# Kernel tuning notes

Measured on AMD Instinct MI355X. Metric: run time of the kernel, lower is better.

The kernel has to match this reference:

```python
import jax, jax.numpy as jnp
import numpy as np

F_IN, U, N_CLS = 256, 512, 50


def _gru_scan(x_tbf, W, Uk, b):
    """Keras GRU (reset_after=True, tanh/sigmoid). x_tbf: [T,B,F]. Returns [T,B,U]."""
    b_in, b_rec = b[0], b[1]                 # each [3U]
    xg = jnp.einsum('tbf,fg->tbg', x_tbf, W) + b_in   # precompute input gates [T,B,3U]
    B = x_tbf.shape[1]
    h0 = jnp.zeros((B, U), dtype=x_tbf.dtype)

    def step(h, xt):
        rec = h @ Uk + b_rec                 # [B,3U]
        xz, xr, xh = jnp.split(xt, 3, axis=-1)
        rz, rr, rh = jnp.split(rec, 3, axis=-1)
        z = jax.nn.sigmoid(xz + rz)
        r = jax.nn.sigmoid(xr + rr)
        hh = jnp.tanh(xh + r * rh)
        h_new = z * h + (1.0 - z) * hh
        return h_new, h_new

    _, ys = jax.lax.scan(step, h0, xg)
    return ys


def setup_inputs() -> dict:
    key = jax.random.key(0)
    ks = jax.random.split(key, 10)
    x = jax.random.normal(ks[0], (32, 1024, F_IN), dtype=jnp.float32)
    # glorot-ish scales
    s_w = (2.0 / (F_IN + 3 * U)) ** 0.5
    s_u = (2.0 / (U + 3 * U)) ** 0.5
    s_d = (2.0 / (2 * U + N_CLS)) ** 0.5
    Wf = jax.random.normal(ks[1], (F_IN, 3 * U), dtype=jnp.float32) * s_w
    Uf = jax.random.normal(ks[2], (U, 3 * U), dtype=jnp.float32) * s_u
    bf = jnp.zeros((2, 3 * U), dtype=jnp.float32)
    Wb = jax.random.normal(ks[3], (F_IN, 3 * U), dtype=jnp.float32) * s_w
    Ub = jax.random.normal(ks[4], (U, 3 * U), dtype=jnp.float32) * s_u
    bb = jnp.zeros((2, 3 * U), dtype=jnp.float32)
    Wd = jax.random.normal(ks[5], (2 * U, N_CLS), dtype=jnp.float32) * s_d
    bd = jnp.zeros((N_CLS,), dtype=jnp.float32)
    return {"x": x, "Wf": Wf, "Uf": Uf, "bf": bf, "Wb": Wb, "Ub": Ub, "bb": bb, "Wd": Wd, "bd": bd}


def reference(x, Wf, Uf, bf, Wb, Ub, bb, Wd, bd):
    # training=False -> dropout / recurrent_dropout are identity.
    x_tbf = jnp.transpose(x, (1, 0, 2))                       # [T,B,F]
    fwd = _gru_scan(x_tbf, Wf, Uf, bf)                        # [T,B,U]
    bwd = _gru_scan(x_tbf[::-1], Wb, Ub, bb)[::-1]            # reversed-in, re-reversed out
    h = jnp.concatenate([fwd, bwd], axis=-1)                  # [T,B,2U]
    h = jnp.transpose(h, (1, 0, 2))                           # [B,T,2U]
    logits = jnp.einsum('btd,dc->btc', h, Wd) + bd            # [B,T,50]
    return jax.nn.softmax(logits, axis=-1)
```

## Files before the change

kernel.cpp:

```cpp
#include <hip/hip_runtime.h>
#include <hip/hip_bf16.h>

#define F_IN  256
#define UNITS 512
#define T_SEQ 1024
#define B_SZ  32
#define NCLS  50
#define NG    16
#define NWAVE 6
#define SCOPE __HIP_MEMORY_SCOPE_AGENT

typedef short s16x8 __attribute__((ext_vector_type(8)));
typedef float f32x16 __attribute__((ext_vector_type(16)));

__device__ __forceinline__ ushort f2bf(float f) {
  union { float f; unsigned u; } v; v.f = f;
  unsigned r = v.u + 0x7fffu + ((v.u >> 16) & 1u);
  return (ushort)(r >> 16);
}


__global__ void prep_xT(const float* __restrict__ x, ushort* __restrict__ xT) {
  int idx = blockIdx.x * 256 + threadIdx.x;
  int b = idx >> 15;
  int r = idx & 32767;
  int t = r >> 5;
  int c = r & 31;
  const float4* s4 = (const float4*)(x + ((size_t)b * T_SEQ + t) * F_IN + c * 8);
  float4 f0 = s4[0], f1 = s4[1];
  s16x8 o;
  o[0] = (short)f2bf(f0.x); o[1] = (short)f2bf(f0.y);
  o[2] = (short)f2bf(f0.z); o[3] = (short)f2bf(f0.w);
  o[4] = (short)f2bf(f1.x); o[5] = (short)f2bf(f1.y);
  o[6] = (short)f2bf(f1.z); o[7] = (short)f2bf(f1.w);
  *(s16x8*)(xT + ((size_t)t * B_SZ + b) * F_IN + c * 8) = o;
}

__global__ void prep_UWT(const float* __restrict__ Uf, const float* __restrict__ Wf,
                         const float* __restrict__ Ub, const float* __restrict__ Wb,
                         ushort* __restrict__ UWT) {
  int idx = blockIdx.x * 256 + threadIdx.x;
  int d = idx / 147456;
  int r = idx % 147456;
  int n = r / 96;
  int ck = r % 96;
  const float* U = d ? Ub : Uf;
  const float* W = d ? Wb : Wf;
  s16x8 o;
  #pragma unroll
  for (int i = 0; i < 8; ++i) {
    int k = ck * 8 + i;
    float v = (k < UNITS) ? U[(size_t)k * 1536 + n] : W[(size_t)(k - UNITS) * 1536 + n];
    o[i] = (short)f2bf(v);
  }
  *(s16x8*)(UWT + ((size_t)d * 1536 + n) * 768 + ck * 8) = o;
}

__global__ void prep_WdT(const float* __restrict__ Wd, ushort* __restrict__ WdT) {
  int idx = blockIdx.x * 256 + threadIdx.x;
  int n = idx >> 10, k = idx & 1023;
  float v = (n < NCLS) ? Wd[(size_t)k * NCLS + n] : 0.f;
  WdT[idx] = f2bf(v);
}

__global__ __launch_bounds__(384, 2) void gru_rec(
    const ushort* __restrict__ xT,
    const ushort* __restrict__ UWT,
    const float* __restrict__ bias_f,
    const float* __restrict__ bias_b,
    ushort* __restrict__ h_out,
    unsigned* __restrict__ tags)
{
  const int g  = blockIdx.x;
  const int d  = g >> 4;
  const int gg = g & 15;
  const int tid  = threadIdx.x;
  const int wv   = tid >> 6;
  const int lane = tid & 63;
  const int col  = lane & 31;
  const int half = lane >> 5;
  const int gate = wv >> 1;
  const int kh   = wv & 1;

  __shared__ float slot[2][32][128];

  s16x8 bfrag[24];
  {
    const ushort* bp = UWT + ((size_t)d * 1536 + gate * UNITS + gg * 32 + col) * 768
                       + kh * 384 + half * 8;
    #pragma unroll
    for (int c = 0; c < 24; ++c) bfrag[c] = *(const s16x8*)(bp + c * 16);
  }

  const float* bias = d ? bias_b : bias_f;
  float bz[3], br[3], bih[3], brh[3], hprev[3];
  #pragma unroll
  for (int i = 0; i < 3; ++i) {
    int e = tid + 384 * i;
    int j = gg * 32 + (e & 31);
    bz[i] = br[i] = bih[i] = brh[i] = 0.f;
    hprev[i] = 0.f;
    if (e < 1024) {
      bz[i]  = bias[j]        + bias[1536 + j];
      br[i]  = bias[512 + j]  + bias[1536 + 512 + j];
      bih[i] = bias[1024 + j];
      brh[i] = bias[1536 + 1024 + j];
    }
  }

  for (int s = 0; s < T_SEQ; ++s) {
    const int t_in = d ? (T_SEQ - 1 - s) : s;
    f32x16 acc_a, acc_b;
    #pragma unroll
    for (int i = 0; i < 16; ++i) { acc_a[i] = 0.f; acc_b[i] = 0.f; }

    if (kh) {
      const ushort* xp = xT + ((size_t)t_in * B_SZ + col) * F_IN + half * 8;
      #pragma unroll
      for (int grp = 0; grp < 2; ++grp) {
        s16x8 a[8];
        #pragma unroll
        for (int i = 0; i < 8; ++i) a[i] = *(const s16x8*)(xp + (grp * 8 + i) * 16);
        #pragma unroll
        for (int i = 0; i < 8; ++i)
          acc_b = __builtin_amdgcn_mfma_f32_32x32x16_bf16(a[i], bfrag[8 + grp * 8 + i], acc_b, 0, 0, 0);
      }
    }

    if (s > 0) {
      if (wv == 0) {
        const unsigned expv = (unsigned)s;
        const unsigned* tg = tags + d * NG;
        bool done;
        do {
          unsigned v = (lane < NG)
              ? __hip_atomic_load(tg + lane, __ATOMIC_RELAXED, SCOPE) : expv;
          done = __all(v >= expv);
          if (!done) __builtin_amdgcn_s_sleep(1);
        } while (!done);
      }
      __syncthreads();

      const int t_prev = d ? (T_SEQ - s) : (s - 1);
      const ushort* ap = h_out + ((size_t)(d * T_SEQ + t_prev) * B_SZ + col) * UNITS
                         + kh * 384 + half * 8;
      if (kh) {
        s16x8 a[8];
        #pragma unroll
        for (int i = 0; i < 8; ++i) a[i] = *(const s16x8*)(ap + i * 16);
        #pragma unroll
        for (int i = 0; i < 8; ++i)
          acc_a = __builtin_amdgcn_mfma_f32_32x32x16_bf16(a[i], bfrag[i], acc_a, 0, 0, 0);
      } else {
        #pragma unroll
        for (int grp = 0; grp < 2; ++grp) {
          s16x8 a[12];
          #pragma unroll
          for (int i = 0; i < 12; ++i) a[i] = *(const s16x8*)(ap + (grp * 12 + i) * 16);
          #pragma unroll
          for (int i = 0; i < 12; ++i)
            acc_a = __builtin_amdgcn_mfma_f32_32x32x16_bf16(a[i], bfrag[grp * 12 + i], acc_a, 0, 0, 0);
        }
      }
    }

    #pragma unroll
    for (int i = 0; i < 16; ++i) {
      int brow = (i & 3) + 8 * (i >> 2) + 4 * half;
      if (gate < 2) {
        slot[kh][brow][gate * 32 + col] = acc_a[i] + acc_b[i];
      } else {
        slot[kh][brow][64 + col] = acc_a[i];
        if (kh) slot[1][brow][96 + col] = acc_b[i];
      }
    }
    __syncthreads();

    #pragma unroll
    for (int i = 0; i < 3; ++i) {
      int e = tid + 384 * i;
      if (e < 1024) {
        int b = e >> 5, j = e & 31;
        float rz = slot[0][b][j]      + slot[1][b][j]      + bz[i];
        float rr = slot[0][b][32 + j] + slot[1][b][32 + j] + br[i];
        float rh = slot[0][b][64 + j] + slot[1][b][64 + j] + brh[i];
        float xh = slot[1][b][96 + j] + bih[i];
        rz = fminf(fmaxf(rz, -30.f), 30.f);
        rr = fminf(fmaxf(rr, -30.f), 30.f);
        float z  = 1.f / (1.f + __expf(-rz));
        float rg = 1.f / (1.f + __expf(-rr));
        float ti = xh + rg * rh;
        ti = fminf(fmaxf(ti, -15.f), 15.f);
        float ex = __expf(2.f * ti);
        float hh = (ex - 1.f) / (ex + 1.f);
        float hn = z * hprev[i] + (1.f - z) * hh;
        hprev[i] = hn;
        __hip_atomic_store(
            h_out + ((size_t)(d * T_SEQ + t_in) * B_SZ + b) * UNITS + gg * 32 + j,
            (ushort)f2bf(hn), __ATOMIC_RELAXED, SCOPE);
      }
    }
    __syncthreads();
    if (tid == 0)
      __hip_atomic_store(tags + d * NG + gg, (unsigned)(s + 1),
                         __ATOMIC_RELAXED, SCOPE);
  }
}

__global__ __launch_bounds__(256) void dense_softmax(
    const ushort* __restrict__ h_out,
    const ushort* __restrict__ WdT,
    const float* __restrict__ bd,
    float* __restrict__ out)
{
  const int tid  = threadIdx.x;
  const int w    = tid >> 6, lane = tid & 63;
  const int col  = lane & 31, half = lane >> 5;
  const int t = blockIdx.x * 4 + w;

  __shared__ float lds[4][32][66];

  f32x16 acc0, acc1;
  #pragma unroll
  for (int i = 0; i < 16; ++i) { acc0[i] = 0.f; acc1[i] = 0.f; }

  const ushort* af  = h_out + ((size_t)t * B_SZ + col) * UNITS + half * 8;
  const ushort* ab  = h_out + ((size_t)(T_SEQ + t) * B_SZ + col) * UNITS + half * 8;
  const ushort* bp0 = WdT + (size_t)col * 1024 + half * 8;
  const ushort* bp1 = WdT + (size_t)(col + 32) * 1024 + half * 8;

  #pragma unroll 4
  for (int ks = 0; ks < 64; ++ks) {
    s16x8 a  = (ks < 32) ? *(const s16x8*)(af + ks * 16)
                         : *(const s16x8*)(ab + (ks - 32) * 16);
    s16x8 b0 = *(const s16x8*)(bp0 + ks * 16);
    s16x8 b1 = *(const s16x8*)(bp1 + ks * 16);
    acc0 = __builtin_amdgcn_mfma_f32_32x32x16_bf16(a, b0, acc0, 0, 0, 0);
    acc1 = __builtin_amdgcn_mfma_f32_32x32x16_bf16(a, b1, acc1, 0, 0, 0);
  }

  #pragma unroll
  for (int i = 0; i < 16; ++i) {
    int b = (i & 3) + 8 * (i >> 2) + 4 * half;
    lds[w][b][col]      = acc0[i];
    lds[w][b][32 + col] = acc1[i];
  }
  __syncthreads();

  if (tid < 128) {
    int tl = tid >> 5, b = tid & 31;
    int tt = blockIdx.x * 4 + tl;
    float v[NCLS];
    float m = -1e30f;
    #pragma unroll
    for (int c = 0; c < NCLS; ++c) { v[c] = lds[tl][b][c] + bd[c]; m = fmaxf(m, v[c]); }
    float sum = 0.f;
    #pragma unroll
    for (int c = 0; c < NCLS; ++c) { float e = __expf(v[c] - m); v[c] = e; sum += e; }
    float inv = 1.f / sum;
    float* op = out + ((size_t)b * T_SEQ + tt) * NCLS;
    #pragma unroll
    for (int c = 0; c < NCLS; ++c) op[c] = v[c] * inv;
  }
}

extern "C" void kernel_launch(void* const* d_in, const int* in_sizes, int n_in,
                              void* d_out, int out_size, void* d_ws, size_t ws_size,
                              hipStream_t stream) {
  const float* x  = (const float*)d_in[0];
  const float* Wf = (const float*)d_in[1];
  const float* Uf = (const float*)d_in[2];
  const float* bf = (const float*)d_in[3];
  const float* Wb = (const float*)d_in[4];
  const float* Ub = (const float*)d_in[5];
  const float* bb = (const float*)d_in[6];
  const float* Wd = (const float*)d_in[7];
  const float* bd = (const float*)d_in[8];
  float* out = (float*)d_out;

  char* ws = (char*)d_ws;
  ushort*   xT    = (ushort*)  (ws + 0);
  ushort*   UWT   = (ushort*)  (ws + 16777216);
  ushort*   WdTp  = (ushort*)  (ws + 21495808);
  ushort*   h_buf = (ushort*)  (ws + 21626880);
  unsigned* tags  = (unsigned*)(ws + 88735744);

  hipMemsetAsync(tags, 0, 2 * NG * sizeof(unsigned), stream);
  hipLaunchKernelGGL(prep_xT,       dim3(4096), dim3(256), 0, stream, x, xT);
  hipLaunchKernelGGL(prep_UWT,      dim3(1152), dim3(256), 0, stream, Uf, Wf, Ub, Wb, UWT);
  hipLaunchKernelGGL(prep_WdT,      dim3(256),  dim3(256), 0, stream, Wd, WdTp);
  hipLaunchKernelGGL(gru_rec,       dim3(32),   dim3(384), 0, stream, xT, UWT, bf, bb, h_buf, tags);
  hipLaunchKernelGGL(dense_softmax, dim3(256),  dim3(256), 0, stream, h_buf, WdTp, bd, out);
}
```

Measured before the change: 7.077 ms.

## Pin each GRU direction's blocks to one XCC and split MFMA accumulator chains

The recurrent kernel now launches 512 blocks. Each block reads its hardware XCC ID and claims a slot through an atomic counter, so all 16 forward-direction blocks run on XCC 0 and all 16 backward-direction blocks run on XCC 1. Surplus blocks exit at once. The aim is to keep the per-step tag polling and the hidden-state exchange inside one XCC's L2 instead of crossing dies on every timestep. Each MFMA reduction chain is also split into two independent accumulators to shorten the dependency chain, at the cost of extra registers. The risks are the wasted block launches and a dependence on how the hardware places blocks on XCCs.

```diff
diff --git a/kernel.cpp b/kernel.cpp
--- a/kernel.cpp
+++ b/kernel.cpp
@@ -69,12 +69,28 @@
     const float* __restrict__ bias_f,
     const float* __restrict__ bias_b,
     ushort* __restrict__ h_out,
-    unsigned* __restrict__ tags)
+    unsigned* __restrict__ tags,
+    unsigned* __restrict__ claim)
 {
-  const int g  = blockIdx.x;
-  const int d  = g >> 4;
-  const int gg = g & 15;
   const int tid  = threadIdx.x;
+
+  unsigned xcc;
+  asm volatile("s_getreg_b32 %0, hwreg(HW_REG_XCC_ID)" : "=s"(xcc));
+
+  __shared__ int s_slot;
+  if (tid == 0) {
+    int sl = -1;
+    if (xcc <= 1) {
+      unsigned t = __hip_atomic_fetch_add(&claim[xcc], 1u, __ATOMIC_RELAXED, SCOPE);
+      if (t < NG) sl = (int)(xcc * NG + t);
+    }
+    s_slot = sl;
+  }
+  __syncthreads();
+  if (s_slot < 0) return;
+  const int d  = s_slot >> 4;
+  const int gg = s_slot & 15;
+
   const int wv   = tid >> 6;
   const int lane = tid & 63;
   const int col  = lane & 31;
@@ -110,20 +126,19 @@
 
   for (int s = 0; s < T_SEQ; ++s) {
     const int t_in = d ? (T_SEQ - 1 - s) : s;
-    f32x16 acc_a, acc_b;
-    #pragma unroll
-    for (int i = 0; i < 16; ++i) { acc_a[i] = 0.f; acc_b[i] = 0.f; }
+    f32x16 acc_a, acc_a2, acc_b, acc_b2;
+    #pragma unroll
+    for (int i = 0; i < 16; ++i) { acc_a[i] = 0.f; acc_a2[i] = 0.f; acc_b[i] = 0.f; acc_b2[i] = 0.f; }
 
     if (kh) {
       const ushort* xp = xT + ((size_t)t_in * B_SZ + col) * F_IN + half * 8;
+      s16x8 a[16];
       #pragma unroll
-      for (int grp = 0; grp < 2; ++grp) {
-        s16x8 a[8];
-        #pragma unroll
-        for (int i = 0; i < 8; ++i) a[i] = *(const s16x8*)(xp + (grp * 8 + i) * 16);
-        #pragma unroll
-        for (int i = 0; i < 8; ++i)
-          acc_b = __builtin_amdgcn_mfma_f32_32x32x16_bf16(a[i], bfrag[8 + grp * 8 + i], acc_b, 0, 0, 0);
+      for (int i = 0; i < 16; ++i) a[i] = *(const s16x8*)(xp + i * 16);
+      #pragma unroll
+      for (int i = 0; i < 8; ++i) {
+        acc_b  = __builtin_amdgcn_mfma_f32_32x32x16_bf16(a[2*i],   bfrag[8 + 2*i],   acc_b,  0, 0, 0);
+        acc_b2 = __builtin_amdgcn_mfma_f32_32x32x16_bf16(a[2*i+1], bfrag[8 + 2*i+1], acc_b2, 0, 0, 0);
       }
     }
 
@@ -149,8 +164,10 @@
         #pragma unroll
         for (int i = 0; i < 8; ++i) a[i] = *(const s16x8*)(ap + i * 16);
         #pragma unroll
-        for (int i = 0; i < 8; ++i)
-          acc_a = __builtin_amdgcn_mfma_f32_32x32x16_bf16(a[i], bfrag[i], acc_a, 0, 0, 0);
+        for (int i = 0; i < 4; ++i) {
+          acc_a  = __builtin_amdgcn_mfma_f32_32x32x16_bf16(a[2*i],   bfrag[2*i],   acc_a,  0, 0, 0);
+          acc_a2 = __builtin_amdgcn_mfma_f32_32x32x16_bf16(a[2*i+1], bfrag[2*i+1], acc_a2, 0, 0, 0);
+        }
       } else {
         #pragma unroll
         for (int grp = 0; grp < 2; ++grp) {
@@ -158,8 +175,10 @@
           #pragma unroll
           for (int i = 0; i < 12; ++i) a[i] = *(const s16x8*)(ap + (grp * 12 + i) * 16);
           #pragma unroll
-          for (int i = 0; i < 12; ++i)
-            acc_a = __builtin_amdgcn_mfma_f32_32x32x16_bf16(a[i], bfrag[grp * 12 + i], acc_a, 0, 0, 0);
+          for (int i = 0; i < 6; ++i) {
+            acc_a  = __builtin_amdgcn_mfma_f32_32x32x16_bf16(a[2*i],   bfrag[grp*12 + 2*i],   acc_a,  0, 0, 0);
+            acc_a2 = __builtin_amdgcn_mfma_f32_32x32x16_bf16(a[2*i+1], bfrag[grp*12 + 2*i+1], acc_a2, 0, 0, 0);
+          }
         }
       }
     }
@@ -167,11 +186,13 @@
     #pragma unroll
     for (int i = 0; i < 16; ++i) {
       int brow = (i & 3) + 8 * (i >> 2) + 4 * half;
+      float ra = acc_a[i] + acc_a2[i];
+      float rb = acc_b[i] + acc_b2[i];
       if (gate < 2) {
-        slot[kh][brow][gate * 32 + col] = acc_a[i] + acc_b[i];
+        slot[kh][brow][gate * 32 + col] = ra + rb;
       } else {
-        slot[kh][brow][64 + col] = acc_a[i];
-        if (kh) slot[1][brow][96 + col] = acc_b[i];
+        slot[kh][brow][64 + col] = ra;
+        if (kh) slot[1][brow][96 + col] = rb;
       }
     }
     __syncthreads();
@@ -284,11 +305,12 @@
   ushort*   WdTp  = (ushort*)  (ws + 21495808);
   ushort*   h_buf = (ushort*)  (ws + 21626880);
   unsigned* tags  = (unsigned*)(ws + 88735744);
-
-  hipMemsetAsync(tags, 0, 2 * NG * sizeof(unsigned), stream);
+  unsigned* claim = (unsigned*)(ws + 88735872);
+
+  hipMemsetAsync(tags, 0, 2 * NG * sizeof(unsigned) + 2 * sizeof(unsigned), stream);
   hipLaunchKernelGGL(prep_xT,       dim3(4096), dim3(256), 0, stream, x, xT);
   hipLaunchKernelGGL(prep_UWT,      dim3(1152), dim3(256), 0, stream, Uf, Wf, Ub, Wb, UWT);
   hipLaunchKernelGGL(prep_WdT,      dim3(256),  dim3(256), 0, stream, Wd, WdTp);
-  hipLaunchKernelGGL(gru_rec,       dim3(32),   dim3(384), 0, stream, xT, UWT, bf, bb, h_buf, tags);
+  hipLaunchKernelGGL(gru_rec,       dim3(512),  dim3(384), 0, stream, xT, UWT, bf, bb, h_buf, tags, claim);
   hipLaunchKernelGGL(dense_softmax, dim3(256),  dim3(256), 0, stream, h_buf, WdTp, bd, out);
 }
```

Measured after the change: 7.568 ms. 6.9% more time.

## Precompute input gates and run recurrence in 4 single-block workgroups with LDS hidden state

Applied to the files above, without the earlier changes.

Adds a prep_xg kernel that computes the input-gate projection for all timesteps with MFMA ahead of time. A new gru_rec2 then runs each direction and batch half in one 1024-thread block. Each block keeps its slice of U in registers, exchanges the hidden state through swizzled LDS, and syncs with __syncthreads instead of cross-block tag polling. This removes global inter-block synchronisation per timestep, but uses only 4 CUs and about 200 MB of extra workspace. The old path is kept as a fallback when the workspace is too small.

```diff
diff --git a/kernel.cpp b/kernel.cpp
--- a/kernel.cpp
+++ b/kernel.cpp
@@ -11,6 +11,8 @@
 #define SCOPE __HIP_MEMORY_SCOPE_AGENT
 
 typedef short s16x8 __attribute__((ext_vector_type(8)));
+typedef short s16x4 __attribute__((ext_vector_type(4)));
+typedef float f32x4 __attribute__((ext_vector_type(4)));
 typedef float f32x16 __attribute__((ext_vector_type(16)));
 
 __device__ __forceinline__ ushort f2bf(float f) {
@@ -18,14 +20,200 @@
   unsigned r = v.u + 0x7fffu + ((v.u >> 16) & 1u);
   return (ushort)(r >> 16);
 }
+__device__ __forceinline__ float bf2f(ushort u) {
+  union { unsigned i; float f; } v; v.i = ((unsigned)u) << 16; return v.f;
+}
+
+__global__ void prep_WdT(const float* __restrict__ Wd, ushort* __restrict__ WdT) {
+  int idx = blockIdx.x * 256 + threadIdx.x;
+  int n = idx >> 10, k = idx & 1023;
+  float v = (n < NCLS) ? Wd[(size_t)k * NCLS + n] : 0.f;
+  WdT[idx] = f2bf(v);
+}
+
+
+__global__ void prep_w(const float* __restrict__ Uf, const float* __restrict__ Wf,
+                       const float* __restrict__ Ub, const float* __restrict__ Wb,
+                       ushort* __restrict__ UT, ushort* __restrict__ WT) {
+  int idx = blockIdx.x * 256 + threadIdx.x;
+  int d = idx / (1536 * 768);
+  int r = idx % (1536 * 768);
+  int n = r / 768, k = r % 768;
+  if (k < 512) {
+    const float* U = d ? Ub : Uf;
+    UT[((size_t)d * 1536 + n) * 512 + k] = f2bf(U[(size_t)k * 1536 + n]);
+  } else {
+    const float* W = d ? Wb : Wf;
+    WT[((size_t)d * 1536 + n) * 256 + (k - 512)] = f2bf(W[(size_t)(k - 512) * 1536 + n]);
+  }
+}
+
+__global__ __launch_bounds__(256) void prep_xg(
+    const float* __restrict__ x, const ushort* __restrict__ WT,
+    const float* __restrict__ bias_f, const float* __restrict__ bias_b,
+    ushort* __restrict__ xg)
+{
+  const int T    = blockIdx.x * 4 + (threadIdx.x >> 6);
+  const int lane = threadIdx.x & 63;
+  const int cl   = lane & 15;
+  const int khi  = (lane >> 4) << 3;
+  const int tile = T % 96;
+  const int grp  = (T / 96) & 3;
+  const int t    = T / 384;
+  const int d = grp >> 1, hb = grp & 1;
+
+  const int colg = tile * 16 + cl;
+  const int b    = hb * 16 + cl;
+
+  const float*  xp = x  + ((size_t)b * T_SEQ + t) * F_IN + khi;
+  const ushort* wp = WT + ((size_t)d * 1536 + colg) * 256 + khi;
+
+  f32x4 acc = {0.f, 0.f, 0.f, 0.f};
+  #pragma unroll
+  for (int ks = 0; ks < 8; ++ks) {
+    float4 f0 = *(const float4*)(xp + ks * 32);
+    float4 f1 = *(const float4*)(xp + ks * 32 + 4);
+    s16x8 a;
+    a[0] = (short)f2bf(f0.x); a[1] = (short)f2bf(f0.y);
+    a[2] = (short)f2bf(f0.z); a[3] = (short)f2bf(f0.w);
+    a[4] = (short)f2bf(f1.x); a[5] = (short)f2bf(f1.y);
+    a[6] = (short)f2bf(f1.z); a[7] = (short)f2bf(f1.w);
+    s16x8 w8 = *(const s16x8*)(wp + ks * 32);
+    acc = __builtin_amdgcn_mfma_f32_16x16x32_bf16(a, w8, acc, 0, 0, 0);
+  }
+  const float* bias = d ? bias_b : bias_f;
+  float bv = bias[colg] + (colg < 1024 ? bias[1536 + colg] : 0.f);
+  size_t To = ((size_t)((d * 2 + hb) * 1024 + t)) * 96 + tile;
+  s16x4 o;
+  #pragma unroll
+  for (int i = 0; i < 4; ++i) o[i] = (short)f2bf(acc[i] + bv);
+  *(s16x4*)(xg + (To * 64 + lane) * 4) = o;
+}
+
+__global__ __launch_bounds__(1024, 1) void gru_rec2(
+    const ushort* __restrict__ xg, const ushort* __restrict__ UT,
+    const float* __restrict__ bias_f, const float* __restrict__ bias_b,
+    ushort* __restrict__ h_out)
+{
+  const int d  = blockIdx.x >> 1;
+  const int hb = blockIdx.x & 1;
+  const int tid  = threadIdx.x;
+  const int wv   = tid >> 6;
+  const int lane = tid & 63;
+  const int cl   = lane & 15;
+  const int khi  = (lane >> 4) << 3;
+  const int rowbase = (lane >> 4) << 2;
+
+  __shared__ ushort hl[2][16 * 512];
+
+  {
+    s16x8 z8 = {0, 0, 0, 0, 0, 0, 0, 0};
+    *(s16x8*)(&hl[0][tid * 8]) = z8;
+  }
+
+  s16x8 bf0[2][16], bf1[2][16], bf2[2][16];
+  {
+    const ushort* base = UT + ((size_t)d * 1536) * 512;
+    #pragma unroll
+    for (int u = 0; u < 2; ++u) {
+      const ushort* p0 = base + (size_t)(0 * 512 + wv * 32 + u * 16 + cl) * 512 + khi;
+      const ushort* p1 = base + (size_t)(1 * 512 + wv * 32 + u * 16 + cl) * 512 + khi;
+      const ushort* p2 = base + (size_t)(2 * 512 + wv * 32 + u * 16 + cl) * 512 + khi;
+      #pragma unroll
+      for (int ks = 0; ks < 16; ++ks) {
+        bf0[u][ks] = *(const s16x8*)(p0 + ks * 32);
+        bf1[u][ks] = *(const s16x8*)(p1 + ks * 32);
+        bf2[u][ks] = *(const s16x8*)(p2 + ks * 32);
+      }
+    }
+  }
+
+  const float* bias = d ? bias_b : bias_f;
+  const float brh0 = bias[1536 + 1024 + wv * 32 + cl];
+  const float brh1 = bias[1536 + 1024 + wv * 32 + 16 + cl];
+
+  float hp0[4], hp1[4];
+  #pragma unroll
+  for (int i = 0; i < 4; ++i) { hp0[i] = 0.f; hp1[i] = 0.f; }
+
+  __syncthreads();
+
+  for (int s = 0; s < T_SEQ; ++s) {
+    const int t  = d ? (T_SEQ - 1 - s) : s;
+    const int pb = s & 1;
+    const int cb = pb ^ 1;
+
+    const size_t Tb = ((size_t)((d * 2 + hb) * 1024 + t)) * 96;
+    const size_t lq = (size_t)lane * 4;
+    s16x4 xg00 = *(const s16x4*)(xg + (Tb + 0 * 32 + wv * 2 + 0) * 256 + lq);
+    s16x4 xg01 = *(const s16x4*)(xg + (Tb + 0 * 32 + wv * 2 + 1) * 256 + lq);
+    s16x4 xg10 = *(const s16x4*)(xg + (Tb + 1 * 32 + wv * 2 + 0) * 256 + lq);
+    s16x4 xg11 = *(const s16x4*)(xg + (Tb + 1 * 32 + wv * 2 + 1) * 256 + lq);
+    s16x4 xg20 = *(const s16x4*)(xg + (Tb + 2 * 32 + wv * 2 + 0) * 256 + lq);
+    s16x4 xg21 = *(const s16x4*)(xg + (Tb + 2 * 32 + wv * 2 + 1) * 256 + lq);
+
+    f32x4 az0 = {0.f,0.f,0.f,0.f}, az1 = {0.f,0.f,0.f,0.f};
+    f32x4 ar0 = {0.f,0.f,0.f,0.f}, ar1 = {0.f,0.f,0.f,0.f};
+    f32x4 ah0 = {0.f,0.f,0.f,0.f}, ah1 = {0.f,0.f,0.f,0.f};
+
+    const ushort* hbase = &hl[pb][cl * 512];
+    const int swz = (cl & 7) << 3;
+    #pragma unroll
+    for (int ks = 0; ks < 16; ++ks) {
+      s16x8 a = *(const s16x8*)(hbase + (((ks * 32) + khi) ^ swz));
+      az0 = __builtin_amdgcn_mfma_f32_16x16x32_bf16(a, bf0[0][ks], az0, 0, 0, 0);
+      az1 = __builtin_amdgcn_mfma_f32_16x16x32_bf16(a, bf0[1][ks], az1, 0, 0, 0);
+      ar0 = __builtin_amdgcn_mfma_f32_16x16x32_bf16(a, bf1[0][ks], ar0, 0, 0, 0);
+      ar1 = __builtin_amdgcn_mfma_f32_16x16x32_bf16(a, bf1[1][ks], ar1, 0, 0, 0);
+      ah0 = __builtin_amdgcn_mfma_f32_16x16x32_bf16(a, bf2[0][ks], ah0, 0, 0, 0);
+      ah1 = __builtin_amdgcn_mfma_f32_16x16x32_bf16(a, bf2[1][ks], ah1, 0, 0, 0);
+    }
+
+    ushort* hw = &hl[cb][0];
+    ushort* ho = h_out + ((size_t)(d * T_SEQ + t) * B_SZ + hb * 16) * UNITS;
+    #pragma unroll
+    for (int i = 0; i < 4; ++i) {
+      const int row = rowbase + i;
+      const int rswz = (row & 7) << 3;
+      {
+        float xz = bf2f((ushort)xg00[i]);
+        float xr = bf2f((ushort)xg10[i]);
+        float xh = bf2f((ushort)xg20[i]);
+        float z  = __builtin_amdgcn_rcpf(1.f + __expf(-(az0[i] + xz)));
+        float r  = __builtin_amdgcn_rcpf(1.f + __expf(-(ar0[i] + xr)));
+        float th = xh + r * (ah0[i] + brh0);
+        float hh = 1.f - 2.f * __builtin_amdgcn_rcpf(1.f + __expf(2.f * th));
+        float hn = z * hp0[i] + (1.f - z) * hh;
+        hp0[i] = hn;
+        ushort hv = f2bf(hn);
+        int j = wv * 32 + cl;
+        hw[row * 512 + (j ^ rswz)] = hv;
+        ho[(size_t)row * UNITS + j] = hv;
+      }
+      {
+        float xz = bf2f((ushort)xg01[i]);
+        float xr = bf2f((ushort)xg11[i]);
+        float xh = bf2f((ushort)xg21[i]);
+        float z  = __builtin_amdgcn_rcpf(1.f + __expf(-(az1[i] + xz)));
+        float r  = __builtin_amdgcn_rcpf(1.f + __expf(-(ar1[i] + xr)));
+        float th = xh + r * (ah1[i] + brh1);
+        float hh = 1.f - 2.f * __builtin_amdgcn_rcpf(1.f + __expf(2.f * th));
+        float hn = z * hp1[i] + (1.f - z) * hh;
+        hp1[i] = hn;
+        ushort hv = f2bf(hn);
+        int j = wv * 32 + 16 + cl;
+        hw[row * 512 + (j ^ rswz)] = hv;
+        ho[(size_t)row * UNITS + j] = hv;
+      }
+    }
+    __syncthreads();
+  }
+}
 
 
 __global__ void prep_xT(const float* __restrict__ x, ushort* __restrict__ xT) {
   int idx = blockIdx.x * 256 + threadIdx.x;
-  int b = idx >> 15;
-  int r = idx & 32767;
-  int t = r >> 5;
-  int c = r & 31;
+  int b = idx >> 15; int r = idx & 32767; int t = r >> 5; int c = r & 31;
   const float4* s4 = (const float4*)(x + ((size_t)b * T_SEQ + t) * F_IN + c * 8);
   float4 f0 = s4[0], f1 = s4[1];
   s16x8 o;
@@ -40,10 +228,7 @@
                          const float* __restrict__ Ub, const float* __restrict__ Wb,
                          ushort* __restrict__ UWT) {
   int idx = blockIdx.x * 256 + threadIdx.x;
-  int d = idx / 147456;
-  int r = idx % 147456;
-  int n = r / 96;
-  int ck = r % 96;
+  int d = idx / 147456; int r = idx % 147456; int n = r / 96; int ck = r % 96;
   const float* U = d ? Ub : Uf;
   const float* W = d ? Wb : Wf;
   s16x8 o;
@@ -56,20 +241,10 @@
   *(s16x8*)(UWT + ((size_t)d * 1536 + n) * 768 + ck * 8) = o;
 }
 
-__global__ void prep_WdT(const float* __restrict__ Wd, ushort* __restrict__ WdT) {
-  int idx = blockIdx.x * 256 + threadIdx.x;
-  int n = idx >> 10, k = idx & 1023;
-  float v = (n < NCLS) ? Wd[(size_t)k * NCLS + n] : 0.f;
-  WdT[idx] = f2bf(v);
-}
-
-__global__ __launch_bounds__(384, 2) void gru_rec(
-    const ushort* __restrict__ xT,
-    const ushort* __restrict__ UWT,
-    const float* __restrict__ bias_f,
-    const float* __restrict__ bias_b,
-    ushort* __restrict__ h_out,
-    unsigned* __restrict__ tags)
+__global__ __launch_bounds__(384, 2) void gru_rec_fb(
+    const ushort* __restrict__ xT, const ushort* __restrict__ UWT,
+    const float* __restrict__ bias_f, const float* __restrict__ bias_b,
+    ushort* __restrict__ h_out, unsigned* __restrict__ tags)
 {
   const int g  = blockIdx.x;
   const int d  = g >> 4;
@@ -208,10 +383,8 @@
 }
 
 __global__ __launch_bounds__(256) void dense_softmax(
-    const ushort* __restrict__ h_out,
-    const ushort* __restrict__ WdT,
-    const float* __restrict__ bd,
-    float* __restrict__ out)
+    const ushort* __restrict__ h_out, const ushort* __restrict__ WdT,
+    const float* __restrict__ bd, float* __restrict__ out)
 {
   const int tid  = threadIdx.x;
   const int w    = tid >> 6, lane = tid & 63;
@@ -277,18 +450,32 @@
   const float* Wd = (const float*)d_in[7];
   const float* bd = (const float*)d_in[8];
   float* out = (float*)d_out;
-
   char* ws = (char*)d_ws;
-  ushort*   xT    = (ushort*)  (ws + 0);
-  ushort*   UWT   = (ushort*)  (ws + 16777216);
-  ushort*   WdTp  = (ushort*)  (ws + 21495808);
-  ushort*   h_buf = (ushort*)  (ws + 21626880);
-  unsigned* tags  = (unsigned*)(ws + 88735744);
-
-  hipMemsetAsync(tags, 0, 2 * NG * sizeof(unsigned), stream);
-  hipLaunchKernelGGL(prep_xT,       dim3(4096), dim3(256), 0, stream, x, xT);
-  hipLaunchKernelGGL(prep_UWT,      dim3(1152), dim3(256), 0, stream, Uf, Wf, Ub, Wb, UWT);
-  hipLaunchKernelGGL(prep_WdT,      dim3(256),  dim3(256), 0, stream, Wd, WdTp);
-  hipLaunchKernelGGL(gru_rec,       dim3(32),   dim3(384), 0, stream, xT, UWT, bf, bb, h_buf, tags);
-  hipLaunchKernelGGL(dense_softmax, dim3(256),  dim3(256), 0, stream, h_buf, WdTp, bd, out);
-}
+
+  if (ws_size >= 273285120ULL) {
+    ushort* UT    = (ushort*)(ws + 0);
+    ushort* WT    = (ushort*)(ws + 3145728);
+    ushort* WdTp  = (ushort*)(ws + 4718592);
+    ushort* h_buf = (ushort*)(ws + 4849664);
+    ushort* xg    = (ushort*)(ws + 71958528);
+
+    hipLaunchKernelGGL(prep_w,        dim3(9216),  dim3(256),  0, stream, Uf, Wf, Ub, Wb, UT, WT);
+    hipLaunchKernelGGL(prep_WdT,      dim3(256),   dim3(256),  0, stream, Wd, WdTp);
+    hipLaunchKernelGGL(prep_xg,       dim3(98304), dim3(256),  0, stream, x, WT, bf, bb, xg);
+    hipLaunchKernelGGL(gru_rec2,      dim3(4),     dim3(1024), 0, stream, xg, UT, bf, bb, h_buf);
+    hipLaunchKernelGGL(dense_softmax, dim3(256),   dim3(256),  0, stream, h_buf, WdTp, bd, out);
+  } else {
+    ushort*   xT    = (ushort*)  (ws + 0);
+    ushort*   UWT   = (ushort*)  (ws + 16777216);
+    ushort*   WdTp  = (ushort*)  (ws + 21495808);
+    ushort*   h_buf = (ushort*)  (ws + 21626880);
+    unsigned* tags  = (unsigned*)(ws + 88735744);
+
+    hipMemsetAsync(tags, 0, 2 * NG * sizeof(unsigned), stream);
+    hipLaunchKernelGGL(prep_xT,       dim3(4096), dim3(256), 0, stream, x, xT);
+    hipLaunchKernelGGL(prep_UWT,      dim3(1152), dim3(256), 0, stream, Uf, Wf, Ub, Wb, UWT);
+    hipLaunchKernelGGL(prep_WdT,      dim3(256),  dim3(256), 0, stream, Wd, WdTp);
+    hipLaunchKernelGGL(gru_rec_fb,    dim3(32),   dim3(384), 0, stream, xT, UWT, bf, bb, h_buf, tags);
+    hipLaunchKernelGGL(dense_softmax, dim3(256),  dim3(256), 0, stream, h_buf, WdTp, bd, out);
+  }
+}
```

Result: no change. 7.095 ms (+0.2%).
